# Performance work log

Hardware: AMD Instinct MI355X
Metric: run time of the kernel (lower is better)

The kernel has to match this reference:

```python
import jax, jax.numpy as jnp
import numpy as np

H = 32   # hidden_dim
D = 3    # input_dim
NM, NF = 16, 64
ME, FE = 4, 2


def setup_inputs() -> dict:
    key = jax.random.key(0)
    ks = jax.random.split(key, 12)
    B, T = 16384, 1024
    s_ih = 1.0 / np.sqrt(H)
    inp = {
        "x": jax.random.normal(ks[0], (B, T, D), dtype=jnp.float32),
        "mat_idx": jax.random.randint(ks[1], (B,), 0, NM, dtype=jnp.int32),
        "freq_idx": jax.random.randint(ks[2], (B,), 0, NF, dtype=jnp.int32),
        # LSTM params (PyTorch layout: gates [i, f, g, o] stacked)
        "W_ih": jax.random.uniform(ks[3], (4 * H, D), jnp.float32, -s_ih, s_ih),
        "W_hh": jax.random.uniform(ks[4], (4 * H, H), jnp.float32, -s_ih, s_ih),
        "b_ih": jax.random.uniform(ks[5], (4 * H,), jnp.float32, -s_ih, s_ih),
        "b_hh": jax.random.uniform(ks[6], (4 * H,), jnp.float32, -s_ih, s_ih),
        "mat_emb": jax.random.normal(ks[7], (NM, ME), dtype=jnp.float32),
        "freq_emb": jax.random.normal(ks[8], (NF, FE), dtype=jnp.float32),
        "fc_w": jax.random.uniform(ks[9], (1, H + ME + FE), jnp.float32, -s_ih, s_ih),
        "fc_b": jax.random.uniform(ks[10], (1,), jnp.float32, -s_ih, s_ih),
    }
    return inp


def _lstm_last(x, W_ih, W_hh, b_ih, b_hh):
    # x: [B, T, D] -> last hidden state h_T: [B, H]
    B = x.shape[0]
    # Precompute input projections for all timesteps: [T, B, 4H]
    xg = jnp.einsum("btd,gd->tbg", x, W_ih) + (b_ih + b_hh)

    def step(carry, xg_t):
        h, c = carry
        gates = xg_t + h @ W_hh.T  # [B, 4H]
        i, f, g, o = jnp.split(gates, 4, axis=-1)
        i, f, o = jax.nn.sigmoid(i), jax.nn.sigmoid(f), jax.nn.sigmoid(o)
        g = jnp.tanh(g)
        c = f * c + i * g
        h = o * jnp.tanh(c)
        return (h, c), None

    h0 = jnp.zeros((B, H), dtype=x.dtype)
    (h, _), _ = jax.lax.scan(step, (h0, h0), xg)
    return h


def reference(x, mat_idx, freq_idx, W_ih, W_hh, b_ih, b_hh,
              mat_emb, freq_emb, fc_w, fc_b):
    last = _lstm_last(x, W_ih, W_hh, b_ih, b_hh)          # [B, H]
    feat = jnp.concatenate(
        [last, mat_emb[mat_idx], freq_emb[freq_idx]], axis=-1)  # [B, H+ME+FE]
    return (feat @ fc_w.T + fc_b)[:, 0]                   # [B]
```

## Files before the change

kernel.cpp:

```cpp
#include <hip/hip_runtime.h>
#include <hip/hip_bf16.h>

#define H 32
#define DCT 32
#define BT 16
#define HPADB 80
#define XLDS_BYTES (DCT*BT*16)
#define HLDS_OFF XLDS_BYTES
#define HBUF (BT*HPADB)
#define SMEM_BYTES (XLDS_BYTES + 2*HBUF)

typedef __attribute__((ext_vector_type(8))) short bfrag;
typedef __attribute__((ext_vector_type(4))) float ffrag;

__device__ __forceinline__ unsigned short f2bf(float f) {
  union { float f; unsigned u; } v; v.f = f;
  unsigned r = v.u + 0x7FFFu + ((v.u >> 16) & 1u);
  return (unsigned short)(r >> 16);
}

__device__ __forceinline__ float sig_pre(float s) {
  return __builtin_amdgcn_rcpf(1.0f + __builtin_amdgcn_exp2f(s));
}
__device__ __forceinline__ float tanh_pre(float s) {
  return 1.0f - 2.0f * __builtin_amdgcn_rcpf(1.0f + __builtin_amdgcn_exp2f(s));
}

__device__ __forceinline__ void lstm_step(unsigned char* smem,
    unsigned x_off, unsigned rd_off, unsigned wr_off,
    const bfrag* fx, const bfrag* fw, ffrag fzero, float* cc, float* hh)
{
  bfrag ah = *(const bfrag*)(smem + rd_off);
  bfrag ax = *(const bfrag*)(smem + x_off);
  ffrag a0 = __builtin_amdgcn_mfma_f32_16x16x32_bf16(ax, fx[0], fzero, 0,0,0);
  ffrag a1 = __builtin_amdgcn_mfma_f32_16x16x32_bf16(ax, fx[1], fzero, 0,0,0);
  ffrag a2 = __builtin_amdgcn_mfma_f32_16x16x32_bf16(ax, fx[2], fzero, 0,0,0);
  ffrag a3 = __builtin_amdgcn_mfma_f32_16x16x32_bf16(ax, fx[3], fzero, 0,0,0);
  a0 = __builtin_amdgcn_mfma_f32_16x16x32_bf16(ah, fw[0], a0, 0,0,0);
  a1 = __builtin_amdgcn_mfma_f32_16x16x32_bf16(ah, fw[1], a1, 0,0,0);
  a2 = __builtin_amdgcn_mfma_f32_16x16x32_bf16(ah, fw[2], a2, 0,0,0);
  a3 = __builtin_amdgcn_mfma_f32_16x16x32_bf16(ah, fw[3], a3, 0,0,0);
  #pragma unroll
  for (int r = 0; r < 4; ++r) {
    float i_ = sig_pre(a0[r]);
    float f_ = sig_pre(a1[r]);
    float tg = tanh_pre(a2[r]);
    float o_ = sig_pre(a3[r]);
    float c  = f_*cc[r] + i_*tg;
    cc[r] = c;
    float h = o_ * tanh_pre(c * 2.885390082f);
    hh[r] = h;
    __hip_bfloat16 hb = __float2bfloat16(h);
    *(unsigned short*)(smem + wr_off + (unsigned)r*HPADB) =
        __builtin_bit_cast(unsigned short, hb);
  }
  __syncthreads();
}

__global__ __launch_bounds__(128, 2) void lstm_kernel(
    const float* __restrict__ x, const int* __restrict__ mat_idx,
    const int* __restrict__ freq_idx, const float* __restrict__ W_ih,
    const float* __restrict__ W_hh, const float* __restrict__ b_ih,
    const float* __restrict__ b_hh, const float* __restrict__ mat_emb,
    const float* __restrict__ freq_emb, const float* __restrict__ fc_w,
    const float* __restrict__ fc_b, float* __restrict__ out, int T)
{
  __shared__ __align__(16) unsigned char smem[SMEM_BYTES];
  const int tid  = threadIdx.x;
  const int lane = tid & 63;
  const int h16  = tid >> 6;
  const int q    = lane >> 4;
  const int c16  = lane & 15;
  const int hid  = h16*16 + c16;
  const int b0   = blockIdx.x * BT;

  for (int i = tid; i < SMEM_BYTES/4; i += 128) ((unsigned*)smem)[i] = 0u;

  bfrag fw[4]; bfrag fx[4];
  #pragma unroll
  for (int g = 0; g < 4; ++g) {
    const float sc = (g == 2) ? 2.885390082f : -1.442695041f;
    const int col = g*H + hid;
    const float* wr = W_hh + col*H + q*8;
    #pragma unroll
    for (int j = 0; j < 8; ++j) fw[g][j] = (short)f2bf(wr[j] * sc);
    #pragma unroll
    for (int j = 0; j < 8; ++j) {
      float v = 0.0f;
      if (q == 0) {
        if (j < 3)       v = W_ih[col*3 + j] * sc;
        else if (j == 3) v = (b_ih[col] + b_hh[col]) * sc;
      }
      fx[g][j] = (short)f2bf(v);
    }
  }

  const unsigned rdA = HLDS_OFF + (unsigned)c16*HPADB + (unsigned)q*16;
  const unsigned rdB = rdA + HBUF;
  const unsigned wrA = HLDS_OFF + (unsigned)(q*4)*HPADB + (unsigned)hid*2;
  const unsigned wrB = wrA + HBUF;
  const unsigned x_rd = (unsigned)c16*16;

  ffrag fzero = {0.f,0.f,0.f,0.f};
  float cc[4] = {0.f,0.f,0.f,0.f};
  float hh[4] = {0.f,0.f,0.f,0.f};

  const int srow = tid >> 3, ssub = tid & 7;
  const float* xsrc = x + (size_t)(b0 + srow) * (size_t)T * 3;

  __syncthreads();

  for (int t0 = 0; t0 < T; t0 += DCT) {
    {
      const float* p = xsrc + (size_t)(t0 + ssub*4) * 3;
      float v[12];
      #pragma unroll
      for (int u = 0; u < 12; ++u) v[u] = p[u];
      #pragma unroll
      for (int u = 0; u < 4; ++u) {
        unsigned w0 = (unsigned)f2bf(v[u*3+0]) | ((unsigned)f2bf(v[u*3+1]) << 16);
        unsigned w1 = (unsigned)f2bf(v[u*3+2]) | (0x3F80u << 16);
        uint2* dst = (uint2*)(smem + (unsigned)((ssub*4+u)*BT + srow)*16);
        *dst = make_uint2(w0, w1);
      }
    }
    __syncthreads();

    #pragma unroll 2
    for (int tl = 0; tl < DCT; tl += 2) {
      lstm_step(smem, x_rd + (unsigned)tl*(BT*16),     rdA, wrB, fx, fw, fzero, cc, hh);
      lstm_step(smem, x_rd + (unsigned)(tl+1)*(BT*16), rdB, wrA, fx, fw, fzero, cc, hh);
    }
  }

  float* hout = (float*)smem;
  #pragma unroll
  for (int r = 0; r < 4; ++r)
    hout[(q*4 + r)*H + hid] = hh[r];
  __syncthreads();
  if (tid < BT) {
    const int b = b0 + tid;
    float acc = fc_b[0];
    const float* hv = hout + tid*H;
    #pragma unroll
    for (int k = 0; k < H; ++k) acc += hv[k]*fc_w[k];
    const int mi = mat_idx[b];
    #pragma unroll
    for (int e = 0; e < 4; ++e) acc += mat_emb[mi*4+e]*fc_w[H+e];
    const int fi = freq_idx[b];
    #pragma unroll
    for (int e = 0; e < 2; ++e) acc += freq_emb[fi*2+e]*fc_w[H+4+e];
    out[b] = acc;
  }
}

extern "C" void kernel_launch(void* const* d_in, const int* in_sizes, int n_in,
                              void* d_out, int out_size, void* d_ws, size_t ws_size,
                              hipStream_t stream) {
  const float* x        = (const float*)d_in[0];
  const int*   mat_idx  = (const int*)d_in[1];
  const int*   freq_idx = (const int*)d_in[2];
  const float* W_ih     = (const float*)d_in[3];
  const float* W_hh     = (const float*)d_in[4];
  const float* b_ih     = (const float*)d_in[5];
  const float* b_hh     = (const float*)d_in[6];
  const float* mat_emb  = (const float*)d_in[7];
  const float* freq_emb = (const float*)d_in[8];
  const float* fc_w     = (const float*)d_in[9];
  const float* fc_b     = (const float*)d_in[10];
  float* out = (float*)d_out;
  const int B = in_sizes[1];
  const int T = in_sizes[0] / (B * 3);
  dim3 grid(B / BT), block(128);
  hipLaunchKernelGGL(lstm_kernel, grid, block, 0, stream,
                     x, mat_idx, freq_idx, W_ih, W_hh, b_ih, b_hh,
                     mat_emb, freq_emb, fc_w, fc_b, out, T);
}
```

Baseline: 889.4 us.

## Use one wavefront per batch tile, drop barriers, and fuse gate nonlinearities algebraically

Each block now has a single 64-lane wavefront that computes all 32 hidden units. It does twice as many MFMAs per lane, so the per-step __syncthreads and the chunk barrier can be removed and LDS ordering relies on intra-wave execution. The gate math is rewritten so the sigmoid/tanh combination uses fewer reciprocals, through a shared denominator and a clamped exp for tanh(c). The final h is read back from the bf16 LDS buffer instead of fp32 registers. In exchange, per-lane register pressure rises, parallelism per CU falls to one wave per block, and the final h is rounded to bf16.

Result: slower. 929.9 us (+4.6%).

```diff
diff --git a/kernel.cpp b/kernel.cpp
--- a/kernel.cpp
+++ b/kernel.cpp
@@ -6,7 +6,7 @@
 #define BT 16
 #define HPADB 80
 #define XLDS_BYTES (DCT*BT*16)
-#define HLDS_OFF XLDS_BYTES
+#define HOFF XLDS_BYTES
 #define HBUF (BT*HPADB)
 #define SMEM_BYTES (XLDS_BYTES + 2*HBUF)
 
@@ -19,45 +19,49 @@
   return (unsigned short)(r >> 16);
 }
 
-__device__ __forceinline__ float sig_pre(float s) {
-  return __builtin_amdgcn_rcpf(1.0f + __builtin_amdgcn_exp2f(s));
-}
-__device__ __forceinline__ float tanh_pre(float s) {
-  return 1.0f - 2.0f * __builtin_amdgcn_rcpf(1.0f + __builtin_amdgcn_exp2f(s));
-}
-
 __device__ __forceinline__ void lstm_step(unsigned char* smem,
     unsigned x_off, unsigned rd_off, unsigned wr_off,
-    const bfrag* fx, const bfrag* fw, ffrag fzero, float* cc, float* hh)
+    const bfrag fx[4][2], const bfrag fw[4][2], ffrag fz, float* cc)
 {
   bfrag ah = *(const bfrag*)(smem + rd_off);
   bfrag ax = *(const bfrag*)(smem + x_off);
-  ffrag a0 = __builtin_amdgcn_mfma_f32_16x16x32_bf16(ax, fx[0], fzero, 0,0,0);
-  ffrag a1 = __builtin_amdgcn_mfma_f32_16x16x32_bf16(ax, fx[1], fzero, 0,0,0);
-  ffrag a2 = __builtin_amdgcn_mfma_f32_16x16x32_bf16(ax, fx[2], fzero, 0,0,0);
-  ffrag a3 = __builtin_amdgcn_mfma_f32_16x16x32_bf16(ax, fx[3], fzero, 0,0,0);
-  a0 = __builtin_amdgcn_mfma_f32_16x16x32_bf16(ah, fw[0], a0, 0,0,0);
-  a1 = __builtin_amdgcn_mfma_f32_16x16x32_bf16(ah, fw[1], a1, 0,0,0);
-  a2 = __builtin_amdgcn_mfma_f32_16x16x32_bf16(ah, fw[2], a2, 0,0,0);
-  a3 = __builtin_amdgcn_mfma_f32_16x16x32_bf16(ah, fw[3], a3, 0,0,0);
+  ffrag acc[4][2];
   #pragma unroll
-  for (int r = 0; r < 4; ++r) {
-    float i_ = sig_pre(a0[r]);
-    float f_ = sig_pre(a1[r]);
-    float tg = tanh_pre(a2[r]);
-    float o_ = sig_pre(a3[r]);
-    float c  = f_*cc[r] + i_*tg;
-    cc[r] = c;
-    float h = o_ * tanh_pre(c * 2.885390082f);
-    hh[r] = h;
-    __hip_bfloat16 hb = __float2bfloat16(h);
-    *(unsigned short*)(smem + wr_off + (unsigned)r*HPADB) =
-        __builtin_bit_cast(unsigned short, hb);
+  for (int g = 0; g < 4; ++g)
+    #pragma unroll
+    for (int ht = 0; ht < 2; ++ht)
+      acc[g][ht] = __builtin_amdgcn_mfma_f32_16x16x32_bf16(ax, fx[g][ht], fz, 0,0,0);
+  #pragma unroll
+  for (int g = 0; g < 4; ++g)
+    #pragma unroll
+    for (int ht = 0; ht < 2; ++ht)
+      acc[g][ht] = __builtin_amdgcn_mfma_f32_16x16x32_bf16(ah, fw[g][ht], acc[g][ht], 0,0,0);
+
+  #pragma unroll
+  for (int ht = 0; ht < 2; ++ht) {
+    #pragma unroll
+    for (int r = 0; r < 4; ++r) {
+      float I = __builtin_amdgcn_exp2f(acc[0][ht][r]);
+      float F = __builtin_amdgcn_exp2f(acc[1][ht][r]);
+      float G = __builtin_amdgcn_exp2f(acc[2][ht][r]);
+      float A = __builtin_amdgcn_exp2f(acc[3][ht][r]);
+      float Ip1 = I + 1.0f, Fp1 = F + 1.0f;
+      float Gp1 = G + 1.0f, Gm1 = G - 1.0f, Ap1 = A + 1.0f;
+      float t1  = Ip1 * Gp1;
+      float num = cc[ht*4+r] * t1 + Gm1 * Fp1;
+      float den = Fp1 * t1;
+      float c   = num * __builtin_amdgcn_rcpf(den);
+      cc[ht*4+r] = c;
+      float carg = fminf(c * 2.885390082f, 110.0f);
+      float E   = __builtin_amdgcn_exp2f(carg);
+      float h   = (E - 1.0f) * __builtin_amdgcn_rcpf(Ap1 * (E + 1.0f));
+      *(unsigned short*)(smem + wr_off + (unsigned)r*HPADB + (unsigned)ht*32) =
+          f2bf(h);
+    }
   }
-  __syncthreads();
 }
 
-__global__ __launch_bounds__(128, 2) void lstm_kernel(
+__global__ __launch_bounds__(64, 1) void lstm_kernel(
     const float* __restrict__ x, const int* __restrict__ mat_idx,
     const int* __restrict__ freq_idx, const float* __restrict__ W_ih,
     const float* __restrict__ W_hh, const float* __restrict__ b_ih,
@@ -66,84 +70,79 @@
     const float* __restrict__ fc_b, float* __restrict__ out, int T)
 {
   __shared__ __align__(16) unsigned char smem[SMEM_BYTES];
-  const int tid  = threadIdx.x;
-  const int lane = tid & 63;
-  const int h16  = tid >> 6;
-  const int q    = lane >> 4;
-  const int c16  = lane & 15;
-  const int hid  = h16*16 + c16;
-  const int b0   = blockIdx.x * BT;
+  const int tid = threadIdx.x;
+  const int q   = tid >> 4;
+  const int c16 = tid & 15;
+  const int b0  = blockIdx.x * BT;
 
-  for (int i = tid; i < SMEM_BYTES/4; i += 128) ((unsigned*)smem)[i] = 0u;
+  for (int i = tid; i < SMEM_BYTES/4; i += 64) ((unsigned*)smem)[i] = 0u;
 
-  bfrag fw[4]; bfrag fx[4];
+  bfrag fw[4][2]; bfrag fx[4][2];
   #pragma unroll
   for (int g = 0; g < 4; ++g) {
     const float sc = (g == 2) ? 2.885390082f : -1.442695041f;
-    const int col = g*H + hid;
-    const float* wr = W_hh + col*H + q*8;
     #pragma unroll
-    for (int j = 0; j < 8; ++j) fw[g][j] = (short)f2bf(wr[j] * sc);
-    #pragma unroll
-    for (int j = 0; j < 8; ++j) {
-      float v = 0.0f;
-      if (q == 0) {
-        if (j < 3)       v = W_ih[col*3 + j] * sc;
-        else if (j == 3) v = (b_ih[col] + b_hh[col]) * sc;
+    for (int ht = 0; ht < 2; ++ht) {
+      const int col = g*H + ht*16 + c16;
+      const float* wr = W_hh + col*H + q*8;
+      #pragma unroll
+      for (int j = 0; j < 8; ++j) fw[g][ht][j] = (short)f2bf(wr[j] * sc);
+      #pragma unroll
+      for (int j = 0; j < 8; ++j) {
+        float v = 0.0f;
+        if (q == 0) {
+          if (j < 3)       v = W_ih[col*3 + j] * sc;
+          else if (j == 3) v = (b_ih[col] + b_hh[col]) * sc;
+        }
+        fx[g][ht][j] = (short)f2bf(v);
       }
-      fx[g][j] = (short)f2bf(v);
     }
   }
 
-  const unsigned rdA = HLDS_OFF + (unsigned)c16*HPADB + (unsigned)q*16;
-  const unsigned rdB = rdA + HBUF;
-  const unsigned wrA = HLDS_OFF + (unsigned)(q*4)*HPADB + (unsigned)hid*2;
-  const unsigned wrB = wrA + HBUF;
+  const unsigned rd0 = HOFF + (unsigned)c16*HPADB + (unsigned)q*16;
+  const unsigned rd1 = rd0 + HBUF;
+  const unsigned wr0 = HOFF + (unsigned)(q*4)*HPADB + (unsigned)c16*2;
+  const unsigned wr1 = wr0 + HBUF;
   const unsigned x_rd = (unsigned)c16*16;
 
-  ffrag fzero = {0.f,0.f,0.f,0.f};
-  float cc[4] = {0.f,0.f,0.f,0.f};
-  float hh[4] = {0.f,0.f,0.f,0.f};
+  ffrag fz = {0.f,0.f,0.f,0.f};
+  float cc[8] = {0.f,0.f,0.f,0.f,0.f,0.f,0.f,0.f};
 
-  const int srow = tid >> 3, ssub = tid & 7;
-  const float* xsrc = x + (size_t)(b0 + srow) * (size_t)T * 3;
-
-  __syncthreads();
+  const int srow = tid & 15, ssub = tid >> 4;
+  const float* xrow = x + (size_t)(b0 + srow) * (size_t)T * 3;
 
   for (int t0 = 0; t0 < T; t0 += DCT) {
     {
-      const float* p = xsrc + (size_t)(t0 + ssub*4) * 3;
-      float v[12];
+      const float4* p = (const float4*)(xrow + (size_t)(t0 + ssub*8) * 3);
+      float4 v4[6];
       #pragma unroll
-      for (int u = 0; u < 12; ++u) v[u] = p[u];
+      for (int u = 0; u < 6; ++u) v4[u] = p[u];
+      const float* v = (const float*)v4;
       #pragma unroll
-      for (int u = 0; u < 4; ++u) {
+      for (int u = 0; u < 8; ++u) {
         unsigned w0 = (unsigned)f2bf(v[u*3+0]) | ((unsigned)f2bf(v[u*3+1]) << 16);
         unsigned w1 = (unsigned)f2bf(v[u*3+2]) | (0x3F80u << 16);
-        uint2* dst = (uint2*)(smem + (unsigned)((ssub*4+u)*BT + srow)*16);
-        *dst = make_uint2(w0, w1);
+        *(uint2*)(smem + (unsigned)((ssub*8+u)*BT + srow)*16) = make_uint2(w0, w1);
       }
     }
-    __syncthreads();
 
     #pragma unroll 2
     for (int tl = 0; tl < DCT; tl += 2) {
-      lstm_step(smem, x_rd + (unsigned)tl*(BT*16),     rdA, wrB, fx, fw, fzero, cc, hh);
-      lstm_step(smem, x_rd + (unsigned)(tl+1)*(BT*16), rdB, wrA, fx, fw, fzero, cc, hh);
+      lstm_step(smem, x_rd + (unsigned)tl*(BT*16),     rd0, wr1, fx, fw, fz, cc);
+      lstm_step(smem, x_rd + (unsigned)(tl+1)*(BT*16), rd1, wr0, fx, fw, fz, cc);
     }
   }
 
-  float* hout = (float*)smem;
-  #pragma unroll
-  for (int r = 0; r < 4; ++r)
-    hout[(q*4 + r)*H + hid] = hh[r];
   __syncthreads();
   if (tid < BT) {
     const int b = b0 + tid;
     float acc = fc_b[0];
-    const float* hv = hout + tid*H;
+    const unsigned short* hr = (const unsigned short*)(smem + HOFF + (unsigned)tid*HPADB);
     #pragma unroll
-    for (int k = 0; k < H; ++k) acc += hv[k]*fc_w[k];
+    for (int k = 0; k < H; ++k) {
+      union { unsigned u; float f; } cv; cv.u = (unsigned)hr[k] << 16;
+      acc += cv.f * fc_w[k];
+    }
     const int mi = mat_idx[b];
     #pragma unroll
     for (int e = 0; e < 4; ++e) acc += mat_emb[mi*4+e]*fc_w[H+e];
@@ -171,7 +170,7 @@
   float* out = (float*)d_out;
   const int B = in_sizes[1];
   const int T = in_sizes[0] / (B * 3);
-  dim3 grid(B / BT), block(128);
+  dim3 grid(B / BT), block(64);
   hipLaunchKernelGGL(lstm_kernel, grid, block, 0, stream,
                      x, mat_idx, freq_idx, W_ih, W_hh, b_ih, b_hh,
                      mat_emb, freq_emb, fc_w, fc_b, out, T);
```
